# Kernel optimization log

Hardware: AMD Instinct MI355X
Metric: run time of the kernel (lower is better)

## Reference

```python
import jax, jax.numpy as jnp
import numpy as np

EPS = 1e-5

def _layernorm(x, gamma, beta):
    mu = jnp.mean(x, axis=-1, keepdims=True)
    var = jnp.var(x, axis=-1, keepdims=True)
    return (x - mu) * jax.lax.rsqrt(var + EPS) * gamma + beta

def setup_inputs() -> dict:
    key = jax.random.key(0)
    ks = jax.random.split(key, 6)
    B, S, N, c_m, c_z, H, c = 1, 512, 384, 64, 128, 8, 32
    return {
        "m_si": jax.random.normal(ks[0], (B, S, N, c_m), dtype=jnp.float32),
        "z_ij": jax.random.normal(ks[1], (B, N, N, c_z), dtype=jnp.float32),
        "gamma_m": jnp.ones((c_m,), dtype=jnp.float32),
        "beta_m": jnp.zeros((c_m,), dtype=jnp.float32),
        "W1": jax.random.normal(ks[2], (c_m, c * H), dtype=jnp.float32) * 0.05,
        "gamma_z": jnp.ones((c_z,), dtype=jnp.float32),
        "beta_z": jnp.zeros((c_z,), dtype=jnp.float32),
        "W2": jax.random.normal(ks[3], (c_z, H), dtype=jnp.float32) * 0.05,
        "W3": jax.random.normal(ks[4], (c_m, c * H), dtype=jnp.float32) * 0.05,
        "W4": jax.random.normal(ks[5], (c * H, c_m), dtype=jnp.float32) * 0.05,
    }

def reference(m_si, z_ij, gamma_m, beta_m, W1, gamma_z, beta_z, W2, W3, W4):
    B, S, N, c_m = m_si.shape
    H = W2.shape[-1]
    c = W1.shape[-1] // H
    m = _layernorm(m_si, gamma_m, beta_m)                 # [B,S,N,c_m]
    v = (m @ W1).reshape(B, S, N, H, c)                   # values  [B,S,N,H,c]
    g = jax.nn.sigmoid(m @ W3).reshape(B, S, N, H, c)     # gates   [B,S,N,H,c]
    b = _layernorm(z_ij, gamma_z, beta_z) @ W2            # pair bias [B,i,j,H]
    # original: softmax over dim=-2 of [B,H,i,j] i.e. over the i axis
    w = jax.nn.softmax(b, axis=1)                         # [B,i,j,H]
    # broadcast weighted average over tokens, shared across N_msa
    o = g * jnp.einsum('bijh,bsjhc->bsihc', w, v)         # [B,S,N,H,c]
    return o.reshape(B, S, N, H * c) @ W4                 # [B,S,N,c_m]
```

## Files before the change

kernel.cpp:

```cpp
#include <hip/hip_runtime.h>
#include <hip/hip_bf16.h>
#include <math.h>


typedef __attribute__((ext_vector_type(8))) short bf16x8;
typedef __attribute__((ext_vector_type(4))) float f32x4;
typedef unsigned int u32;

__global__ __launch_bounds__(256) void k0_prep(
    const float* __restrict__ W4, const float* __restrict__ W1,
    const float* __restrict__ W3,
    __hip_bfloat16* __restrict__ W4t,
    __hip_bfloat16* __restrict__ W13s)
{
    int idx = blockIdx.x * 256 + threadIdx.x;
    if (idx < 16384) {
        int d = idx >> 8, k = idx & 255;
        W4t[idx] = __float2bfloat16(W4[k * 64 + d]);
    } else {
        int t = idx - 16384;
        int n = t >> 6, k = t & 63;
        float v = (n < 256) ? W1[k * 256 + n] : W3[k * 256 + (n - 256)];
        int dst = n * 64 + ((((k >> 3) ^ (n & 7))) << 3) + (k & 7);
        W13s[dst] = __float2bfloat16(v);
    }
}

__global__ __launch_bounds__(256) void k1_ln_mv(
    const float* __restrict__ m_si,
    const float* __restrict__ gamma_m, const float* __restrict__ beta_m,
    const __hip_bfloat16* __restrict__ W13s,
    __hip_bfloat16* __restrict__ v_tg,
    __hip_bfloat16* __restrict__ g_bf)
{
    __shared__ short a_t[128 * 64];
    __shared__ short b_t[512 * 64];
    const int bx = blockIdx.x;
    const int s = bx / 3, j0 = (bx % 3) * 128;
    const int tid = threadIdx.x;
    const int lane = tid & 63, wv = tid >> 6;
    const int col = lane & 15, quad = lane >> 4;

    {
        const short* src = (const short*)W13s;
        #pragma unroll
        for (int i = 0; i < 16; i++) {
            __builtin_amdgcn_global_load_lds(
                (const __attribute__((address_space(1))) u32*)
                    (src + i * 2048 + wv * 512 + lane * 8),
                (__attribute__((address_space(3))) u32*)(b_t + i * 2048 + wv * 512),
                16, 0, 0);
        }
    }

    {
        const float gm = gamma_m[lane], bm = beta_m[lane];
        const float* mrow = m_si + (size_t)(s * 384 + j0) * 64;
        const int cl = lane >> 3, e = lane & 7;
        #pragma unroll 4
        for (int rr = 0; rr < 32; rr++) {
            int r = wv * 32 + rr;
            float x = mrow[r * 64 + lane];
            float s1 = x, s2 = x * x;
            #pragma unroll
            for (int off = 32; off > 0; off >>= 1) {
                s1 += __shfl_xor(s1, off, 64);
                s2 += __shfl_xor(s2, off, 64);
            }
            float mu  = s1 * (1.0f / 64.0f);
            float var = s2 * (1.0f / 64.0f) - mu * mu;
            float rs  = rsqrtf(var + 1e-5f);
            __hip_bfloat16 mh = __float2bfloat16((x - mu) * rs * gm + bm);
            a_t[r * 64 + ((cl ^ (r & 7)) << 3) + e] = *(short*)&mh;
        }
    }
    __syncthreads();

    const int wm = wv >> 1, wn = wv & 1;

    bf16x8 mf[4][2];
    #pragma unroll
    for (int mt = 0; mt < 4; mt++) {
        int r = wm * 64 + mt * 16 + col;
        #pragma unroll
        for (int ks = 0; ks < 2; ks++) {
            int c = ks * 4 + quad;
            mf[mt][ks] = *(const bf16x8*)&a_t[r * 64 + ((c ^ (r & 7)) << 3)];
        }
    }

    short* vbase = (short*)v_tg + (size_t)s * 98304;
    __hip_bfloat16* gb = g_bf + (size_t)s * 98304;

    #pragma unroll 1
    for (int step = 0; step < 4; step++) {
        bf16x8 wf[4][2];
        #pragma unroll
        for (int nt = 0; nt < 4; nt++) {
            int n = step * 128 + wn * 64 + nt * 16 + col;
            #pragma unroll
            for (int ks = 0; ks < 2; ks++) {
                int c = ks * 4 + quad;
                wf[nt][ks] = *(const bf16x8*)&b_t[n * 64 + ((c ^ (n & 7)) << 3)];
            }
        }

        if (step < 2) {
            f32x4 acc[4][4];
            #pragma unroll
            for (int nt = 0; nt < 4; nt++)
                #pragma unroll
                for (int mt = 0; mt < 4; mt++)
                    acc[nt][mt] = (f32x4){0.f, 0.f, 0.f, 0.f};
            #pragma unroll
            for (int ks = 0; ks < 2; ks++)
                #pragma unroll
                for (int nt = 0; nt < 4; nt++)
                    #pragma unroll
                    for (int mt = 0; mt < 4; mt++)
                        acc[nt][mt] = __builtin_amdgcn_mfma_f32_16x16x32_bf16(
                            wf[nt][ks], mf[mt][ks], acc[nt][mt], 0, 0, 0);
            #pragma unroll
            for (int nt = 0; nt < 4; nt++)
                #pragma unroll
                for (int mt = 0; mt < 4; mt++) {
                    int jg = j0 + wm * 64 + mt * 16 + col;
                    #pragma unroll
                    for (int reg = 0; reg < 4; reg++) {
                        int n = step * 128 + wn * 64 + nt * 16 + quad * 4 + reg;
                        __hip_bfloat16 t = __float2bfloat16(acc[nt][mt][reg]);
                        vbase[n * 384 + jg] = *(short*)&t;
                    }
                }
        } else {
            f32x4 acc[4][4];
            #pragma unroll
            for (int mt = 0; mt < 4; mt++)
                #pragma unroll
                for (int nt = 0; nt < 4; nt++)
                    acc[mt][nt] = (f32x4){0.f, 0.f, 0.f, 0.f};
            #pragma unroll
            for (int ks = 0; ks < 2; ks++)
                #pragma unroll
                for (int mt = 0; mt < 4; mt++)
                    #pragma unroll
                    for (int nt = 0; nt < 4; nt++)
                        acc[mt][nt] = __builtin_amdgcn_mfma_f32_16x16x32_bf16(
                            mf[mt][ks], wf[nt][ks], acc[mt][nt], 0, 0, 0);
            #pragma unroll
            for (int mt = 0; mt < 4; mt++)
                #pragma unroll
                for (int nt = 0; nt < 4; nt++) {
                    int n = (step - 2) * 128 + wn * 64 + nt * 16 + col;
                    #pragma unroll
                    for (int reg = 0; reg < 4; reg++) {
                        int jg = j0 + wm * 64 + mt * 16 + quad * 4 + reg;
                        float gv = 1.0f / (1.0f + __expf(-acc[mt][nt][reg]));
                        gb[(size_t)jg * 256 + n] = __float2bfloat16(gv);
                    }
                }
        }
    }
}

__global__ __launch_bounds__(256) void k2_ln_z(
    const float* __restrict__ z,
    const float* __restrict__ gamma_z, const float* __restrict__ beta_z,
    const float* __restrict__ W2, float* __restrict__ b_buf)
{
    const int tid = threadIdx.x;
    const int lane = tid & 63, wv = tid >> 6;
    const int R0 = blockIdx.x * 64;
    __shared__ float part[64][9];

    float2 g2 = *(const float2*)&gamma_z[lane * 2];
    float2 be2 = *(const float2*)&beta_z[lane * 2];
    float4 w2a = *(const float4*)&W2[lane * 16];
    float4 w2b = *(const float4*)&W2[lane * 16 + 4];
    float4 w2c = *(const float4*)&W2[lane * 16 + 8];
    float4 w2d = *(const float4*)&W2[lane * 16 + 12];

    const bool hi4 = (lane & 4) != 0;
    const bool hi2 = (lane & 2) != 0;
    const bool hi1 = (lane & 1) != 0;

    float2 zx = *(const float2*)&z[(size_t)(R0 + wv * 16) * 128 + lane * 2];
    #pragma unroll 1
    for (int rr = 0; rr < 16; rr++) {
        const int rl = wv * 16 + rr;
        float x0 = zx.x, x1 = zx.y;
        if (rr < 15)
            zx = *(const float2*)&z[(size_t)(R0 + rl + 1) * 128 + lane * 2];

        float s1 = x0 + x1, s2 = x0 * x0 + x1 * x1;
        #pragma unroll
        for (int off = 32; off > 0; off >>= 1) {
            s1 += __shfl_xor(s1, off, 64);
            s2 += __shfl_xor(s2, off, 64);
        }
        float mu  = s1 * (1.0f / 128.0f);
        float var = s2 * (1.0f / 128.0f) - mu * mu;
        float rs  = rsqrtf(var + 1e-5f);
        float mh0 = (x0 - mu) * rs * g2.x + be2.x;
        float mh1 = (x1 - mu) * rs * g2.y + be2.y;

        float p[8];
        p[0] = fmaf(mh0, w2a.x, mh1 * w2c.x);
        p[1] = fmaf(mh0, w2a.y, mh1 * w2c.y);
        p[2] = fmaf(mh0, w2a.z, mh1 * w2c.z);
        p[3] = fmaf(mh0, w2a.w, mh1 * w2c.w);
        p[4] = fmaf(mh0, w2b.x, mh1 * w2d.x);
        p[5] = fmaf(mh0, w2b.y, mh1 * w2d.y);
        p[6] = fmaf(mh0, w2b.z, mh1 * w2d.z);
        p[7] = fmaf(mh0, w2b.w, mh1 * w2d.w);

        float t[4];
        #pragma unroll
        for (int k = 0; k < 4; k++) {
            float keep = hi4 ? p[k + 4] : p[k];
            float send = hi4 ? p[k] : p[k + 4];
            t[k] = keep + __shfl_xor(send, 4, 64);
        }
        float u[2];
        #pragma unroll
        for (int k = 0; k < 2; k++) {
            float keep = hi2 ? t[k + 2] : t[k];
            float send = hi2 ? t[k] : t[k + 2];
            u[k] = keep + __shfl_xor(send, 2, 64);
        }
        float vsum;
        {
            float keep = hi1 ? u[1] : u[0];
            float send = hi1 ? u[0] : u[1];
            vsum = keep + __shfl_xor(send, 1, 64);
        }
        vsum += __shfl_xor(vsum, 8, 64);
        vsum += __shfl_xor(vsum, 16, 64);
        vsum += __shfl_xor(vsum, 32, 64);
        if (lane < 8) part[rl][lane] = vsum;
    }
    __syncthreads();

    {
        int h0 = tid >> 6, rl = tid & 63;
        b_buf[(size_t)h0 * 147456 + R0 + rl]       = part[rl][h0];
        b_buf[(size_t)(h0 + 4) * 147456 + R0 + rl] = part[rl][h0 + 4];
    }
}

__global__ __launch_bounds__(128) void k3a_part(
    const float* __restrict__ w_buf, float* __restrict__ pm, float* __restrict__ pl)
{
    const int h = blockIdx.x / 24, ic = blockIdx.x % 24;
    const int i0 = ic * 16;
    const int tid = threadIdx.x;
    const float* base = w_buf + ((size_t)h * 384 + i0) * 384;

    float m0 = -INFINITY, m1 = -INFINITY, m2 = -INFINITY;
    float l0 = 0.f, l1 = 0.f, l2 = 0.f;
    #pragma unroll 4
    for (int ii = 0; ii < 16; ii++) {
        float x0 = base[ii * 384 + tid];
        float x1 = base[ii * 384 + tid + 128];
        float x2 = base[ii * 384 + tid + 256];
        float n0 = fmaxf(m0, x0);
        l0 = l0 * __expf(m0 - n0) + __expf(x0 - n0); m0 = n0;
        float n1 = fmaxf(m1, x1);
        l1 = l1 * __expf(m1 - n1) + __expf(x1 - n1); m1 = n1;
        float n2 = fmaxf(m2, x2);
        l2 = l2 * __expf(m2 - n2) + __expf(x2 - n2); m2 = n2;
    }
    float* pmb = pm + ((size_t)h * 24 + ic) * 384;
    float* plb = pl + ((size_t)h * 24 + ic) * 384;
    pmb[tid]       = m0;  plb[tid]       = l0;
    pmb[tid + 128] = m1;  plb[tid + 128] = l1;
    pmb[tid + 256] = m2;  plb[tid + 256] = l2;
}

__global__ __launch_bounds__(384) void k3m_comb(
    const float* __restrict__ pm, const float* __restrict__ pl,
    float* __restrict__ Mf, float* __restrict__ invLf)
{
    const int h = blockIdx.x, j = threadIdx.x;
    float M = -INFINITY, L = 0.f;
    #pragma unroll 4
    for (int ic = 0; ic < 24; ic++) {
        float m = pm[((size_t)h * 24 + ic) * 384 + j];
        float l = pl[((size_t)h * 24 + ic) * 384 + j];
        float nM = fmaxf(M, m);
        L = L * __expf(M - nM) + l * __expf(m - nM);
        M = nM;
    }
    Mf[h * 384 + j] = M;
    invLf[h * 384 + j] = 1.0f / L;
}

__global__ __launch_bounds__(128) void k3b_write(
    const float* __restrict__ w_buf, const float* __restrict__ Mf,
    const float* __restrict__ invLf, __hip_bfloat16* __restrict__ w_bf)
{
    const int h = blockIdx.x / 24, ic = blockIdx.x % 24;
    const int i0 = ic * 16;
    const int tid = threadIdx.x;
    const float* base = w_buf + ((size_t)h * 384 + i0) * 384;
    __hip_bfloat16* ob = w_bf + ((size_t)h * 384 + i0) * 384;

    float M0 = Mf[h * 384 + tid],       iL0 = invLf[h * 384 + tid];
    float M1 = Mf[h * 384 + tid + 128], iL1 = invLf[h * 384 + tid + 128];
    float M2 = Mf[h * 384 + tid + 256], iL2 = invLf[h * 384 + tid + 256];
    #pragma unroll 4
    for (int ii = 0; ii < 16; ii++) {
        float x0 = base[ii * 384 + tid];
        float x1 = base[ii * 384 + tid + 128];
        float x2 = base[ii * 384 + tid + 256];
        ob[ii * 384 + tid]       = __float2bfloat16(__expf(x0 - M0) * iL0);
        ob[ii * 384 + tid + 128] = __float2bfloat16(__expf(x1 - M1) * iL1);
        ob[ii * 384 + tid + 256] = __float2bfloat16(__expf(x2 - M2) * iL2);
    }
}

#define OSTR 264

__global__ __launch_bounds__(256, 2) void k4_mfma(
    const __hip_bfloat16* __restrict__ w_bf,
    const __hip_bfloat16* __restrict__ v_tg,
    const __hip_bfloat16* __restrict__ g_bf,
    const __hip_bfloat16* __restrict__ W4t,
    float* __restrict__ out)
{
    __shared__ short v_t[3][6144];
    __shared__ short o_l[64 * OSTR];
    const int bx0 = blockIdx.x;
    const int bx = (bx0 & 7) * 384 + (bx0 >> 3);
    const int s = bx / 6, i0 = (bx % 6) * 64;
    const int tid = threadIdx.x;
    const int lane = tid & 63, wv = tid >> 6;
    const int col = lane & 15, quad = lane >> 4;
    const int swz = col & 7;

    int srow[3], skc[3];
    #pragma unroll
    for (int r = 0; r < 3; r++) {
        int p = r * 256 + tid;
        int row = p / 48;
        srow[r] = row;
        skc[r] = (p - row * 48) ^ (row & 7);
    }

    const short* wA_base = (const short*)w_bf
        + (size_t)(i0 + wv * 16 + col) * 384 + quad * 8;
    const short* vslab = (const short*)v_tg + (size_t)s * 98304;
    const __hip_bfloat16* gbase = g_bf + (size_t)(s * 384 + i0) * 256;
    const int ibase = wv * 16 + quad * 4;

    auto STAGE = [&](int buf, int hh, int half) {
        const short* src = vslab + hh * 12288 + half * 6144;
        short* dstb = &v_t[buf][wv * 512];
        #pragma unroll
        for (int r = 0; r < 3; r++) {
            __builtin_amdgcn_global_load_lds(
                (const __attribute__((address_space(1))) u32*)
                    (src + srow[r] * 384 + skc[r] * 8),
                (__attribute__((address_space(3))) u32*)(dstb + r * 2048),
                16, 0, 0);
        }
    };

    STAGE(0, 0, 0);
    STAGE(1, 0, 1);

    int cb = 0;
    int sb = 2;

    #pragma unroll 1
    for (int h = 0; h < 8; h++) {
        asm volatile("s_waitcnt vmcnt(3)" ::: "memory");
        __builtin_amdgcn_s_barrier();
        __builtin_amdgcn_sched_barrier(0);

        bf16x8 af[12];
        const short* wA = wA_base + (size_t)h * 147456;
        #pragma unroll
        for (int ks = 0; ks < 12; ks++)
            af[ks] = *(const bf16x8*)(wA + ks * 32);

        if (h < 7) { STAGE(sb, h + 1, 0); sb = (sb == 2) ? 0 : sb + 1; }

        f32x4 acc0 = {0.f, 0.f, 0.f, 0.f};
        #pragma unroll
        for (int ks = 0; ks < 12; ks++) {
            int ch = (ks * 4 + quad) ^ swz;
            bf16x8 b = *(const bf16x8*)&v_t[cb][col * 384 + ch * 8];
            acc0 = __builtin_amdgcn_mfma_f32_16x16x32_bf16(af[ks], b, acc0, 0, 0, 0);
        }
        cb = (cb == 2) ? 0 : cb + 1;

        if (h < 7) asm volatile("s_waitcnt vmcnt(3)" ::: "memory");
        else       asm volatile("s_waitcnt vmcnt(0)" ::: "memory");
        __builtin_amdgcn_s_barrier();
        __builtin_amdgcn_sched_barrier(0);

        float g0[4], g1[4];
        #pragma unroll
        for (int reg = 0; reg < 4; reg++) {
            int il = ibase + reg;
            g0[reg] = __bfloat162float(gbase[il * 256 + h * 32 + col]);
            g1[reg] = __bfloat162float(gbase[il * 256 + h * 32 + 16 + col]);
        }

        if (h < 7) { STAGE(sb, h + 1, 1); sb = (sb == 2) ? 0 : sb + 1; }

        f32x4 acc1 = {0.f, 0.f, 0.f, 0.f};
        #pragma unroll
        for (int ks = 0; ks < 12; ks++) {
            int ch = (ks * 4 + quad) ^ swz;
            bf16x8 b = *(const bf16x8*)&v_t[cb][col * 384 + ch * 8];
            acc1 = __builtin_amdgcn_mfma_f32_16x16x32_bf16(af[ks], b, acc1, 0, 0, 0);
        }
        cb = (cb == 2) ? 0 : cb + 1;

        #pragma unroll
        for (int reg = 0; reg < 4; reg++) {
            int il = ibase + reg;
            __hip_bfloat16 t0 = __float2bfloat16(acc0[reg] * g0[reg]);
            __hip_bfloat16 t1 = __float2bfloat16(acc1[reg] * g1[reg]);
            o_l[il * OSTR + h * 32 + col]      = *(short*)&t0;
            o_l[il * OSTR + h * 32 + 16 + col] = *(short*)&t1;
        }
    }

    f32x4 acc2[4];
    #pragma unroll
    for (int n = 0; n < 4; n++) acc2[n] = (f32x4){0.f, 0.f, 0.f, 0.f};
    #pragma unroll
    for (int ks = 0; ks < 8; ks++) {
        int k0 = ks * 32;
        bf16x8 a = *(const bf16x8*)&o_l[(wv * 16 + col) * OSTR + k0 + quad * 8];
        #pragma unroll
        for (int n = 0; n < 4; n++) {
            bf16x8 b = *(const bf16x8*)((const short*)W4t
                        + (n * 16 + col) * 256 + k0 + quad * 8);
            acc2[n] = __builtin_amdgcn_mfma_f32_16x16x32_bf16(a, b, acc2[n], 0, 0, 0);
        }
    }
    float* obase = out + (size_t)(s * 384 + i0 + wv * 16 + quad * 4) * 64;
    #pragma unroll
    for (int n = 0; n < 4; n++)
        #pragma unroll
        for (int reg = 0; reg < 4; reg++)
            obase[reg * 64 + n * 16 + col] = acc2[n][reg];
}

extern "C" void kernel_launch(void* const* d_in, const int* in_sizes, int n_in,
                              void* d_out, int out_size, void* d_ws, size_t ws_size,
                              hipStream_t stream)
{
    const float* m_si    = (const float*)d_in[0];
    const float* z_ij    = (const float*)d_in[1];
    const float* gamma_m = (const float*)d_in[2];
    const float* beta_m  = (const float*)d_in[3];
    const float* W1      = (const float*)d_in[4];
    const float* gamma_z = (const float*)d_in[5];
    const float* beta_z  = (const float*)d_in[6];
    const float* W2      = (const float*)d_in[7];
    const float* W3      = (const float*)d_in[8];
    const float* W4      = (const float*)d_in[9];
    float* out = (float*)d_out;

    char* ws = (char*)d_ws;
    __hip_bfloat16* g_bf = (__hip_bfloat16*)ws;
    __hip_bfloat16* v_tg = (__hip_bfloat16*)(ws + 100663296);
    float*          w_buf = (float*)(ws + 201326592);
    __hip_bfloat16* W13s = (__hip_bfloat16*)(ws + 201326592);
    __hip_bfloat16* w_bf = (__hip_bfloat16*)(ws + 206045184);
    __hip_bfloat16* W4t  = (__hip_bfloat16*)(ws + 208404480);
    float* pm    = (float*)(ws + 208437248);
    float* pl    = (float*)(ws + 208732160);
    float* Mf    = (float*)(ws + 209027072);
    float* invLf = (float*)(ws + 209039360);

    k0_prep  <<<192,  256, 0, stream>>>(W4, W1, W3, W4t, W13s);
    k1_ln_mv <<<1536, 256, 0, stream>>>(m_si, gamma_m, beta_m, W13s, v_tg, g_bf);
    k2_ln_z  <<<2304, 256, 0, stream>>>(z_ij, gamma_z, beta_z, W2, w_buf);
    k3a_part <<<192,  128, 0, stream>>>(w_buf, pm, pl);
    k3m_comb <<<8,    384, 0, stream>>>(pm, pl, Mf, invLf);
    k3b_write<<<192,  128, 0, stream>>>(w_buf, Mf, invLf, w_bf);
    k4_mfma  <<<3072, 256, 0, stream>>>(w_bf, v_tg, g_bf, W4t, out);
}
```

Baseline: 524.5 us.

## Keep gated output in registers and feed W4 GEMM directly via permuted layouts

```diff
diff --git a/kernel.cpp b/kernel.cpp
--- a/kernel.cpp
+++ b/kernel.cpp
@@ -7,16 +7,24 @@
 typedef __attribute__((ext_vector_type(4))) float f32x4;
 typedef unsigned int u32;
 
+__device__ inline float b2f(short v) {
+    union { float f; u32 u; } t; t.u = ((u32)(unsigned short)v) << 16; return t.f;
+}
+
 __global__ __launch_bounds__(256) void k0_prep(
     const float* __restrict__ W4, const float* __restrict__ W1,
     const float* __restrict__ W3,
-    __hip_bfloat16* __restrict__ W4t,
+    __hip_bfloat16* __restrict__ W4p,
     __hip_bfloat16* __restrict__ W13s)
 {
     int idx = blockIdx.x * 256 + threadIdx.x;
     if (idx < 16384) {
         int d = idx >> 8, k = idx & 255;
-        W4t[idx] = __float2bfloat16(W4[k * 64 + d]);
+        int koff = k & 31, h = k >> 5;
+        int quad = koff >> 3, e = koff & 7;
+        int c = (e < 4) ? (quad * 4 + e) : (16 + quad * 4 + (e - 4));
+        int hc = h * 32 + c;
+        W4p[idx] = __float2bfloat16(W4[hc * 64 + d]);
     } else {
         int t = idx - 16384;
         int n = t >> 6, k = t & 63;
@@ -31,7 +39,7 @@
     const float* __restrict__ gamma_m, const float* __restrict__ beta_m,
     const __hip_bfloat16* __restrict__ W13s,
     __hip_bfloat16* __restrict__ v_tg,
-    __hip_bfloat16* __restrict__ g_bf)
+    __hip_bfloat16* __restrict__ g_p)
 {
     __shared__ short a_t[128 * 64];
     __shared__ short b_t[512 * 64];
@@ -90,7 +98,7 @@
     }
 
     short* vbase = (short*)v_tg + (size_t)s * 98304;
-    __hip_bfloat16* gb = g_bf + (size_t)s * 98304;
+    __hip_bfloat16* gb = g_p + (size_t)s * 98304;
 
     #pragma unroll 1
     for (int step = 0; step < 4; step++) {
@@ -152,11 +160,15 @@
                 #pragma unroll
                 for (int nt = 0; nt < 4; nt++) {
                     int n = (step - 2) * 128 + wn * 64 + nt * 16 + col;
+                    int c32 = n & 31;
+                    int koff = ((c32 & 15) >> 2) * 8 + (c32 & 3)
+                             + ((c32 & 16) ? 4 : 0);
+                    int kn = (n & ~31) | koff;
                     #pragma unroll
                     for (int reg = 0; reg < 4; reg++) {
                         int jg = j0 + wm * 64 + mt * 16 + quad * 4 + reg;
                         float gv = 1.0f / (1.0f + __expf(-acc[mt][nt][reg]));
-                        gb[(size_t)jg * 256 + n] = __float2bfloat16(gv);
+                        gb[(size_t)jg * 256 + kn] = __float2bfloat16(gv);
                     }
                 }
         }
@@ -319,17 +331,14 @@
     }
 }
 
-#define OSTR 264
-
-__global__ __launch_bounds__(256, 2) void k4_mfma(
+__global__ __launch_bounds__(256, 3) void k4_mfma(
     const __hip_bfloat16* __restrict__ w_bf,
     const __hip_bfloat16* __restrict__ v_tg,
-    const __hip_bfloat16* __restrict__ g_bf,
-    const __hip_bfloat16* __restrict__ W4t,
+    const __hip_bfloat16* __restrict__ g_p,
+    const __hip_bfloat16* __restrict__ W4p,
     float* __restrict__ out)
 {
-    __shared__ short v_t[3][6144];
-    __shared__ short o_l[64 * OSTR];
+    __shared__ short v_t[2][12288];
     const int bx0 = blockIdx.x;
     const int bx = (bx0 & 7) * 384 + (bx0 >> 3);
     const int s = bx / 6, i0 = (bx % 6) * 64;
@@ -338,94 +347,88 @@
     const int col = lane & 15, quad = lane >> 4;
     const int swz = col & 7;
 
-    int srow[3], skc[3];
-    #pragma unroll
-    for (int r = 0; r < 3; r++) {
+    int srow[6], skc[6];
+    #pragma unroll
+    for (int r = 0; r < 6; r++) {
         int p = r * 256 + tid;
         int row = p / 48;
         srow[r] = row;
         skc[r] = (p - row * 48) ^ (row & 7);
     }
 
-    const short* wA_base = (const short*)w_bf
+    const short* vslab = (const short*)v_tg + (size_t)s * 98304;
+    const short* wbase = (const short*)w_bf
         + (size_t)(i0 + wv * 16 + col) * 384 + quad * 8;
-    const short* vslab = (const short*)v_tg + (size_t)s * 98304;
-    const __hip_bfloat16* gbase = g_bf + (size_t)(s * 384 + i0) * 256;
-    const int ibase = wv * 16 + quad * 4;
-
-    auto STAGE = [&](int buf, int hh, int half) {
-        const short* src = vslab + hh * 12288 + half * 6144;
-        short* dstb = &v_t[buf][wv * 512];
-        #pragma unroll
-        for (int r = 0; r < 3; r++) {
+
+    auto STAGE = [&](int buf, int hh) {
+        const short* src = vslab + hh * 12288;
+        #pragma unroll
+        for (int r = 0; r < 6; r++) {
             __builtin_amdgcn_global_load_lds(
                 (const __attribute__((address_space(1))) u32*)
                     (src + srow[r] * 384 + skc[r] * 8),
-                (__attribute__((address_space(3))) u32*)(dstb + r * 2048),
+                (__attribute__((address_space(3))) u32*)
+                    (&v_t[buf][r * 2048 + wv * 512]),
                 16, 0, 0);
         }
     };
 
-    STAGE(0, 0, 0);
-    STAGE(1, 0, 1);
-
-    int cb = 0;
-    int sb = 2;
-
-    #pragma unroll 1
+    const short* gbase = (const short*)g_p
+        + (size_t)(s * 384 + i0 + wv * 16 + col) * 256 + quad * 8;
+    bf16x8 gf[8];
+    #pragma unroll
+    for (int h = 0; h < 8; h++)
+        gf[h] = *(const bf16x8*)(gbase + h * 32);
+
+    STAGE(0, 0);
+
+    f32x4 acc[8][2];
+    #pragma unroll
     for (int h = 0; h < 8; h++) {
-        asm volatile("s_waitcnt vmcnt(3)" ::: "memory");
+        acc[h][0] = (f32x4){0.f, 0.f, 0.f, 0.f};
+        acc[h][1] = (f32x4){0.f, 0.f, 0.f, 0.f};
+    }
+
+    #pragma unroll
+    for (int h = 0; h < 8; h++) {
+        __builtin_amdgcn_sched_barrier(0);
+        asm volatile("s_waitcnt vmcnt(0)" ::: "memory");
         __builtin_amdgcn_s_barrier();
         __builtin_amdgcn_sched_barrier(0);
 
-        bf16x8 af[12];
-        const short* wA = wA_base + (size_t)h * 147456;
+        bf16x8 wf[12];
+        const short* wA = wbase + (size_t)h * 147456;
         #pragma unroll
         for (int ks = 0; ks < 12; ks++)
-            af[ks] = *(const bf16x8*)(wA + ks * 32);
-
-        if (h < 7) { STAGE(sb, h + 1, 0); sb = (sb == 2) ? 0 : sb + 1; }
-
-        f32x4 acc0 = {0.f, 0.f, 0.f, 0.f};
+            wf[ks] = *(const bf16x8*)(wA + ks * 32);
+
+        if (h < 7) STAGE((h + 1) & 1, h + 1);
+
+        __builtin_amdgcn_s_setprio(1);
         #pragma unroll
         for (int ks = 0; ks < 12; ks++) {
             int ch = (ks * 4 + quad) ^ swz;
-            bf16x8 b = *(const bf16x8*)&v_t[cb][col * 384 + ch * 8];
-            acc0 = __builtin_amdgcn_mfma_f32_16x16x32_bf16(af[ks], b, acc0, 0, 0, 0);
-        }
-        cb = (cb == 2) ? 0 : cb + 1;
-
-        if (h < 7) asm volatile("s_waitcnt vmcnt(3)" ::: "memory");
-        else       asm volatile("s_waitcnt vmcnt(0)" ::: "memory");
-        __builtin_amdgcn_s_barrier();
-        __builtin_amdgcn_sched_barrier(0);
-
-        float g0[4], g1[4];
-        #pragma unroll
-        for (int reg = 0; reg < 4; reg++) {
-            int il = ibase + reg;
-            g0[reg] = __bfloat162float(gbase[il * 256 + h * 32 + col]);
-            g1[reg] = __bfloat162float(gbase[il * 256 + h * 32 + 16 + col]);
-        }
-
-        if (h < 7) { STAGE(sb, h + 1, 1); sb = (sb == 2) ? 0 : sb + 1; }
-
-        f32x4 acc1 = {0.f, 0.f, 0.f, 0.f};
-        #pragma unroll
-        for (int ks = 0; ks < 12; ks++) {
-            int ch = (ks * 4 + quad) ^ swz;
-            bf16x8 b = *(const bf16x8*)&v_t[cb][col * 384 + ch * 8];
-            acc1 = __builtin_amdgcn_mfma_f32_16x16x32_bf16(af[ks], b, acc1, 0, 0, 0);
-        }
-        cb = (cb == 2) ? 0 : cb + 1;
-
-        #pragma unroll
-        for (int reg = 0; reg < 4; reg++) {
-            int il = ibase + reg;
-            __hip_bfloat16 t0 = __float2bfloat16(acc0[reg] * g0[reg]);
-            __hip_bfloat16 t1 = __float2bfloat16(acc1[reg] * g1[reg]);
-            o_l[il * OSTR + h * 32 + col]      = *(short*)&t0;
-            o_l[il * OSTR + h * 32 + 16 + col] = *(short*)&t1;
+            bf16x8 a0 = *(const bf16x8*)&v_t[h & 1][col * 384 + ch * 8];
+            bf16x8 a1 = *(const bf16x8*)&v_t[h & 1][(16 + col) * 384 + ch * 8];
+            acc[h][0] = __builtin_amdgcn_mfma_f32_16x16x32_bf16(
+                            a0, wf[ks], acc[h][0], 0, 0, 0);
+            acc[h][1] = __builtin_amdgcn_mfma_f32_16x16x32_bf16(
+                            a1, wf[ks], acc[h][1], 0, 0, 0);
+        }
+        __builtin_amdgcn_s_setprio(0);
+    }
+
+    bf16x8 paf[8];
+    #pragma unroll
+    for (int h = 0; h < 8; h++) {
+        #pragma unroll
+        for (int e = 0; e < 4; e++) {
+            float v0 = acc[h][0][e] * b2f(gf[h][e]);
+            float v1 = acc[h][1][e] * b2f(gf[h][4 + e]);
+            __hip_bfloat16 t0 = __float2bfloat16(v0);
+            __hip_bfloat16 t1 = __float2bfloat16(v1);
+            paf[h][e]     = *(short*)&t0;
+            paf[h][4 + e] = *(short*)&t1;
         }
     }
 
@@ -433,14 +436,13 @@
     #pragma unroll
     for (int n = 0; n < 4; n++) acc2[n] = (f32x4){0.f, 0.f, 0.f, 0.f};
     #pragma unroll
-    for (int ks = 0; ks < 8; ks++) {
-        int k0 = ks * 32;
-        bf16x8 a = *(const bf16x8*)&o_l[(wv * 16 + col) * OSTR + k0 + quad * 8];
+    for (int h = 0; h < 8; h++) {
         #pragma unroll
         for (int n = 0; n < 4; n++) {
-            bf16x8 b = *(const bf16x8*)((const short*)W4t
-                        + (n * 16 + col) * 256 + k0 + quad * 8);
-            acc2[n] = __builtin_amdgcn_mfma_f32_16x16x32_bf16(a, b, acc2[n], 0, 0, 0);
+            bf16x8 b = *(const bf16x8*)((const short*)W4p
+                        + (n * 16 + col) * 256 + h * 32 + quad * 8);
+            acc2[n] = __builtin_amdgcn_mfma_f32_16x16x32_bf16(
+                          paf[h], b, acc2[n], 0, 0, 0);
         }
     }
     float* obase = out + (size_t)(s * 384 + i0 + wv * 16 + quad * 4) * 64;
@@ -468,22 +470,22 @@
     float* out = (float*)d_out;
 
     char* ws = (char*)d_ws;
-    __hip_bfloat16* g_bf = (__hip_bfloat16*)ws;
+    __hip_bfloat16* g_p  = (__hip_bfloat16*)ws;
     __hip_bfloat16* v_tg = (__hip_bfloat16*)(ws + 100663296);
     float*          w_buf = (float*)(ws + 201326592);
     __hip_bfloat16* W13s = (__hip_bfloat16*)(ws + 201326592);
     __hip_bfloat16* w_bf = (__hip_bfloat16*)(ws + 206045184);
-    __hip_bfloat16* W4t  = (__hip_bfloat16*)(ws + 208404480);
+    __hip_bfloat16* W4p  = (__hip_bfloat16*)(ws + 208404480);
     float* pm    = (float*)(ws + 208437248);
     float* pl    = (float*)(ws + 208732160);
     float* Mf    = (float*)(ws + 209027072);
     float* invLf = (float*)(ws + 209039360);
 
-    k0_prep  <<<192,  256, 0, stream>>>(W4, W1, W3, W4t, W13s);
-    k1_ln_mv <<<1536, 256, 0, stream>>>(m_si, gamma_m, beta_m, W13s, v_tg, g_bf);
+    k0_prep  <<<192,  256, 0, stream>>>(W4, W1, W3, W4p, W13s);
+    k1_ln_mv <<<1536, 256, 0, stream>>>(m_si, gamma_m, beta_m, W13s, v_tg, g_p);
     k2_ln_z  <<<2304, 256, 0, stream>>>(z_ij, gamma_z, beta_z, W2, w_buf);
     k3a_part <<<192,  128, 0, stream>>>(w_buf, pm, pl);
     k3m_comb <<<8,    384, 0, stream>>>(pm, pl, Mf, invLf);
     k3b_write<<<192,  128, 0, stream>>>(w_buf, Mf, invLf, w_bf);
-    k4_mfma  <<<3072, 256, 0, stream>>>(w_bf, v_tg, g_bf, W4t, out);
-}
+    k4_mfma  <<<3072, 256, 0, stream>>>(w_bf, v_tg, g_p, W4p, out);
+}
```

Result: slower. 550.2 us (+4.9%).
